# Performance work log

Measured on AMD Instinct MI355X. Metric: run time of the kernel, lower is better.

The kernel has to match this reference:

```python
import jax, jax.numpy as jnp
import numpy as np

B, N, M = 64, 1025, 1024          # N = M + 1 (node 0 is the zero-padding node)
TREE_FEAT = 96
QVEC = 95                          # sum(range(10)) + 10*5
IN_CH = TREE_FEAT + 32             # tree features + q_conv output
EPS = 1e-5


def _tree_conv(x, idx, W, b):
    # x: (B, C, N); idx: (B, 3M) child-triple indices into node axis
    g = jnp.take_along_axis(x, idx[:, None, :], axis=2)        # (B, C, 3M)
    Bn, C, L = g.shape
    g = g.reshape(Bn, C, L // 3, 3)                            # (B, C, M, 3)
    out = jnp.einsum('bcmk,ock->bom', g, W) + b[None, :, None] # Conv1d k=3 s=3
    zero = jnp.zeros((Bn, W.shape[0], 1), out.dtype)           # re-prepend zero node
    return jnp.concatenate([zero, out], axis=2)                # (B, O, M+1)


def _tree_norm(x):
    # TreeLayerNorm: per-sample mean/std over (channels, nodes); torch.std is unbiased
    mean = jnp.mean(x, axis=(1, 2), keepdims=True)
    std = jnp.std(x, axis=(1, 2), keepdims=True, ddof=1)
    return (x - mean) / (std + EPS)


def setup_inputs() -> dict:
    key = jax.random.key(0)
    ks = jax.random.split(key, 17)
    p = lambda k, s: jax.random.normal(k, s, dtype=jnp.float32) * 0.05
    return {
        'q_vecs': jax.random.normal(ks[0], (B, QVEC), dtype=jnp.float32),
        'trees': jax.random.normal(ks[1], (B, N, TREE_FEAT), dtype=jnp.float32),
        'idxes': jax.random.randint(ks[2], (B, 3 * M), 0, N),
        # q_conv: Linear(95,64) -> Linear(64,128) -> Linear(128,64) -> Linear(64,32)
        'Wq1': p(ks[3], (QVEC, 64)),  'bq1': jnp.zeros((64,), jnp.float32),
        'Wq2': p(ks[4], (64, 128)),   'bq2': jnp.zeros((128,), jnp.float32),
        'Wq3': p(ks[5], (128, 64)),   'bq3': jnp.zeros((64,), jnp.float32),
        'Wq4': p(ks[6], (64, 32)),    'bq4': jnp.zeros((32,), jnp.float32),
        # tree_conv kernels: (out, in, 3)
        'Wc1': p(ks[7], (512, IN_CH, 3)), 'bc1': jnp.zeros((512,), jnp.float32),
        'Wc2': p(ks[8], (256, 512, 3)),   'bc2': jnp.zeros((256,), jnp.float32),
        'Wc3': p(ks[9], (128, 256, 3)),   'bc3': jnp.zeros((128,), jnp.float32),
    }


def reference(q_vecs, trees, idxes,
              Wq1, bq1, Wq2, bq2, Wq3, bq3, Wq4, bq4,
              Wc1, bc1, Wc2, bc2, Wc3, bc3):
    # q_conv: 4 stacked linears (no nonlinearity between them in the source)
    q = q_vecs @ Wq1 + bq1
    q = q @ Wq2 + bq2
    q = q @ Wq3 + bq3
    q = q @ Wq4 + bq4                                    # (B, 32)

    Bn, Nn = trees.shape[:2]
    q_rep = jnp.broadcast_to(q[:, None, :], (Bn, Nn, q.shape[-1]))
    aug = jnp.concatenate([trees, q_rep], axis=2)        # (B, N, IN_CH)
    x = jnp.transpose(aug, (0, 2, 1))                    # (B, IN_CH, N)

    x = _tree_conv(x, idxes, Wc1, bc1)
    x = jax.nn.leaky_relu(_tree_norm(x), negative_slope=0.01)
    x = _tree_conv(x, idxes, Wc2, bc2)
    x = jax.nn.leaky_relu(_tree_norm(x), negative_slope=0.01)
    x = _tree_conv(x, idxes, Wc3, bc3)
    x = _tree_norm(x)
    return jnp.max(x, axis=2)                            # DynamicPooling -> (B, 128)
```

## Files before the change

kernel.cpp:

```cpp
#include <hip/hip_runtime.h>
#include <hip/hip_bf16.h>

typedef __attribute__((ext_vector_type(8))) short short8;
typedef __attribute__((ext_vector_type(4))) float f32x4;

#define EPSV 1e-5f

__device__ __forceinline__ float bf2f(ushort u){
  union { uint i; float f; } x; x.i = ((uint)u) << 16; return x.f;
}
__device__ __forceinline__ ushort f2bf(float f){
  union { float f; uint i; } x; x.f = f;
  uint r = (x.i + 0x7FFFu + ((x.i >> 16) & 1u)) >> 16;
  return (ushort)r;
}

__global__ void init_kernel(ushort* x1, float* stats, int* maxbuf){
  int i = blockIdx.x * 256 + threadIdx.x;
  if (i < 384)  stats[i] = 0.f;
  if (i < 8192) maxbuf[i] = 0;
  if (i < 32768){ int b = i >> 9, c = i & 511; x1[(size_t)b*1025*512 + c] = 0; }
}

__global__ void zero2_kernel(ushort* x2){
  int i = blockIdx.x * 256 + threadIdx.x;
  int b = i >> 8, c = i & 255;
  x2[(size_t)b*1025*256 + c] = 0;
}

__global__ void qconv_kernel(const float* __restrict__ qv,
    const float* __restrict__ W1, const float* __restrict__ b1,
    const float* __restrict__ W2, const float* __restrict__ b2,
    const float* __restrict__ W3, const float* __restrict__ b3,
    const float* __restrict__ W4, const float* __restrict__ b4,
    float* __restrict__ qout){
  __shared__ float v0[96], h1[64], h2[128], h3[64];
  int b = blockIdx.x, t = threadIdx.x;
  if (t < 95) v0[t] = qv[b*95 + t];
  __syncthreads();
  if (t < 64){ float s = b1[t]; for (int i=0;i<95;i++)  s += v0[i]*W1[i*64 + t];  h1[t]=s; }
  __syncthreads();
  if (t < 128){ float s = b2[t]; for (int i=0;i<64;i++)  s += h1[i]*W2[i*128 + t]; h2[t]=s; }
  __syncthreads();
  if (t < 64){ float s = b3[t]; for (int i=0;i<128;i++) s += h2[i]*W3[i*64 + t];  h3[t]=s; }
  __syncthreads();
  if (t < 32){ float s = b4[t]; for (int i=0;i<64;i++)  s += h3[i]*W4[i*32 + t];  qout[b*32 + t]=s; }
}

__global__ void aug_kernel(const float* __restrict__ trees, const float* __restrict__ q,
                           ushort* __restrict__ aug){
  int n = blockIdx.x;
  int b = blockIdx.y;
  int c = threadIdx.x;
  float v = (c < 96) ? trees[((size_t)b*1025 + n)*96 + c] : q[b*32 + (c - 96)];
  aug[(((size_t)b*1025 + n) << 7) + c] = f2bf(v);
}

__global__ void prepw_kernel(const float* __restrict__ wc, ushort* __restrict__ wt,
                             int O, int C){
  int i = blockIdx.x * 256 + threadIdx.x;
  int total = O * 3 * C;
  if (i >= total) return;
  int o  = i / (3*C);
  int K  = i - o*3*C;
  int kp = K / C;
  int c  = K - kp*C;
  wt[i] = f2bf(wc[(o*C + c)*3 + kp]);
}

template<int CIN, int GY, int TM, bool DO_MAX>
__global__ __launch_bounds__(256) void conv_kernel(
    const ushort* __restrict__ xin, const ushort* __restrict__ wt,
    const float* __restrict__ bias, const int* __restrict__ idxes,
    ushort* __restrict__ xout, float* __restrict__ stats, int* __restrict__ maxbuf){
  constexpr int K3    = 3 * CIN;
  constexpr int NT    = K3 / 32;
  constexpr int LOG2  = (CIN == 128) ? 7 : (CIN == 256) ? 8 : 9;
  constexpr int MT    = 1024 / TM;
  constexpr int MF    = TM / 32;
  constexpr int COUT  = GY * 128;
  constexpr int NWG   = MT * GY * 64;

  const int bid  = blockIdx.x;
  const int wu   = (bid & 7) * (NWG >> 3) + (bid >> 3);
  const int m0   = (wu % MT) * TM;
  const int rest = wu / MT;
  const int o0   = (rest % GY) * 128;
  const int b    = rest / GY;

  const int t = threadIdx.x;
  const int lane = t & 63, wid = t >> 6;
  const int WM = (wid & 1) * (TM/2), WO = (wid >> 1) * 64;
  const int fr = lane & 15, fg = lane >> 4;
  const int fc = (fg ^ ((fr >> 1) & 3)) * 8;

  __shared__ __align__(16) ushort As[2][TM][32];
  __shared__ __align__(16) ushort Bs[2][128][32];
  __shared__ int idx_s[3*TM];

  for (int i = t; i < 3*TM; i += 256) idx_s[i] = idxes[b*3072 + m0*3 + i];
  __syncthreads();

  const int rB = t >> 1, h = t & 1, sxB = (rB >> 1) & 3;
  const int pB0 = ((2*h)     ^ sxB) * 8;
  const int pB1 = ((2*h + 1) ^ sxB) * 8;
  const ushort* wrow = wt + (size_t)(o0 + rB) * K3 + h*16;

  const int rA  = (TM == 128) ? (t >> 1) : (t >> 2);
  const int qA  = (TM == 128) ? 0 : (t & 3);
  const int sxA = (rA >> 1) & 3;
  const int pA0 = (TM == 128) ? (((2*h) ^ sxA) * 8) : (((qA) ^ sxA) * 8);
  const int pA1 = ((2*h + 1) ^ sxA) * 8;
  const int aoff = (TM == 128) ? h*16 : qA*8;
  const int n0 = idx_s[rA*3 + 0], n1 = idx_s[rA*3 + 1], n2 = idx_s[rA*3 + 2];
  const ushort* xb  = xin + (size_t)b * 1025 * CIN;
  const ushort* pA0g = xb + (size_t)n0 * CIN + aoff;
  const ushort* pA1g = xb + (size_t)n1 * CIN + aoff;
  const ushort* pA2g = xb + (size_t)n2 * CIN + aoff;

  uint4 a00, a01, a10, a11, b00, b01, b10, b11;

  auto GLOAD0 = [&](int ch){
    const int k0 = ch * 32;
    const int kp = k0 >> LOG2;
    const int c0 = k0 - (kp << LOG2);
    const ushort* sa = ((kp == 0) ? pA0g : (kp == 1) ? pA1g : pA2g) + c0;
    a00 = *reinterpret_cast<const uint4*>(sa);
    if constexpr (TM == 128) a01 = *reinterpret_cast<const uint4*>(sa + 8);
    const ushort* sb = wrow + k0;
    b00 = *reinterpret_cast<const uint4*>(sb);
    b01 = *reinterpret_cast<const uint4*>(sb + 8);
  };
  auto GLOAD1 = [&](int ch){
    const int k0 = ch * 32;
    const int kp = k0 >> LOG2;
    const int c0 = k0 - (kp << LOG2);
    const ushort* sa = ((kp == 0) ? pA0g : (kp == 1) ? pA1g : pA2g) + c0;
    a10 = *reinterpret_cast<const uint4*>(sa);
    if constexpr (TM == 128) a11 = *reinterpret_cast<const uint4*>(sa + 8);
    const ushort* sb = wrow + k0;
    b10 = *reinterpret_cast<const uint4*>(sb);
    b11 = *reinterpret_cast<const uint4*>(sb + 8);
  };
  auto DSW0 = [&](int bf){
    *reinterpret_cast<uint4*>(&As[bf][rA][pA0]) = a00;
    if constexpr (TM == 128) *reinterpret_cast<uint4*>(&As[bf][rA][pA1]) = a01;
    *reinterpret_cast<uint4*>(&Bs[bf][rB][pB0]) = b00;
    *reinterpret_cast<uint4*>(&Bs[bf][rB][pB1]) = b01;
  };
  auto DSW1 = [&](int bf){
    *reinterpret_cast<uint4*>(&As[bf][rA][pA0]) = a10;
    if constexpr (TM == 128) *reinterpret_cast<uint4*>(&As[bf][rA][pA1]) = a11;
    *reinterpret_cast<uint4*>(&Bs[bf][rB][pB0]) = b10;
    *reinterpret_cast<uint4*>(&Bs[bf][rB][pB1]) = b11;
  };

  f32x4 acc[MF][4] = {};
  auto COMPUTE = [&](int cur){
    short8 af[MF], bf4[4];
    #pragma unroll
    for (int i = 0; i < MF; ++i)
      af[i] = *reinterpret_cast<const short8*>(&As[cur][WM + i*16 + fr][fc]);
    #pragma unroll
    for (int i = 0; i < 4; ++i)
      bf4[i] = *reinterpret_cast<const short8*>(&Bs[cur][WO + i*16 + fr][fc]);
    __builtin_amdgcn_s_setprio(1);
    #pragma unroll
    for (int mf = 0; mf < MF; ++mf)
      #pragma unroll
      for (int nf = 0; nf < 4; ++nf)
        acc[mf][nf] = __builtin_amdgcn_mfma_f32_16x16x32_bf16(af[mf], bf4[nf], acc[mf][nf], 0, 0, 0);
    __builtin_amdgcn_s_setprio(0);
  };

  GLOAD0(0);
  DSW0(0);
  GLOAD1(1);
  __syncthreads();

  for (int ch = 0; ch < NT; ch += 2){
    if (ch + 2 < NT) GLOAD0(ch + 2);
    COMPUTE(0);
    DSW1(1);
    __syncthreads();
    if (ch + 3 < NT) GLOAD1(ch + 3);
    COMPUTE(1);
    if (ch + 2 < NT){
      DSW0(0);
      __syncthreads();
    }
  }

  float bsv[4];
  #pragma unroll
  for (int nf = 0; nf < 4; ++nf) bsv[nf] = bias[o0 + WO + nf*16 + fr];
  float lsum = 0.f, lsq = 0.f;
  float cmax[4] = { -1e30f, -1e30f, -1e30f, -1e30f };
  #pragma unroll
  for (int mf = 0; mf < MF; ++mf)
    #pragma unroll
    for (int nf = 0; nf < 4; ++nf)
      #pragma unroll
      for (int i = 0; i < 4; ++i){
        float v = acc[mf][nf][i] + bsv[nf];
        lsum += v; lsq += v*v;
        if (DO_MAX) cmax[nf] = fmaxf(cmax[nf], v);
        else acc[mf][nf][i] = v;
      }
  #pragma unroll
  for (int off = 1; off < 64; off <<= 1){
    lsum += __shfl_xor(lsum, off);
    lsq  += __shfl_xor(lsq,  off);
  }
  if (lane == 0){
    atomicAdd(&stats[b],      lsum);
    atomicAdd(&stats[64 + b], lsq);
  }
  if (DO_MAX){
    #pragma unroll
    for (int nf = 0; nf < 4; ++nf){
      float v = cmax[nf];
      v = fmaxf(v, __shfl_xor(v, 16));
      v = fmaxf(v, __shfl_xor(v, 32));
      if (lane < 16)
        atomicMax(&maxbuf[b*COUT + o0 + WO + nf*16 + fr], __float_as_int(v));
    }
  } else {
    ushort* orow = xout + ((size_t)(b*1025 + 1 + m0 + WM + fg*4))*COUT + o0 + WO + fr;
    #pragma unroll
    for (int mf = 0; mf < MF; ++mf)
      #pragma unroll
      for (int i = 0; i < 4; ++i){
        ushort* pr = orow + (size_t)(mf*16 + i)*COUT;
        #pragma unroll
        for (int nf = 0; nf < 4; ++nf)
          pr[nf*16] = f2bf(acc[mf][nf][i]);
      }
  }
}

__global__ void norm_kernel(ushort* __restrict__ x, const float* __restrict__ st,
                            float cnt, int nvec_per_b){
  int b = blockIdx.y;
  int j = blockIdx.x * 256 + threadIdx.x;
  if (j >= nvec_per_b) return;
  float sum = st[b], sq = st[64 + b];
  float mean = sum / cnt;
  float var  = fmaxf((sq - sum*sum/cnt) / (cnt - 1.f), 0.f);
  float rs   = 1.f / (sqrtf(var) + EPSV);
  ushort* p = x + ((size_t)b * nvec_per_b + j) * 8;
  union { uint4 v; ushort u[8]; } d;
  d.v = *reinterpret_cast<const uint4*>(p);
  #pragma unroll
  for (int k = 0; k < 8; ++k){
    float f = bf2f(d.u[k]);
    f = (f - mean) * rs;
    f = (f >= 0.f) ? f : 0.01f * f;
    d.u[k] = f2bf(f);
  }
  *reinterpret_cast<uint4*>(p) = d.v;
}

__global__ void final_kernel(const int* __restrict__ maxbuf, const float* __restrict__ st,
                             float* __restrict__ out){
  int i = blockIdx.x * 256 + threadIdx.x;
  int b = i >> 7;
  const float cnt = 131200.f;
  float sum = st[b], sq = st[64 + b];
  float mean = sum / cnt;
  float var  = fmaxf((sq - sum*sum/cnt) / (cnt - 1.f), 0.f);
  float rs   = 1.f / (sqrtf(var) + EPSV);
  out[i] = (__int_as_float(maxbuf[i]) - mean) * rs;
}

static constexpr size_t SZ_X1  = (size_t)64*1025*512*2;
static constexpr size_t SZ_X2  = (size_t)64*1025*256*2;
static constexpr size_t OFF_X1 = 0;
static constexpr size_t OFF_X2 = OFF_X1 + SZ_X1;
static constexpr size_t OFF_AUG = OFF_X2;
static constexpr size_t OFF_WT1 = OFF_X2 + SZ_X2;
static constexpr size_t OFF_WT2 = OFF_WT1 + (size_t)512*384*2;
static constexpr size_t OFF_WT3 = OFF_WT2 + (size_t)256*1536*2;
static constexpr size_t OFF_Q   = OFF_WT3 + (size_t)128*768*2;
static constexpr size_t OFF_ST  = OFF_Q + (size_t)64*32*4;
static constexpr size_t OFF_MAX = OFF_ST + (size_t)384*4;

extern "C" void kernel_launch(void* const* d_in, const int* in_sizes, int n_in,
                              void* d_out, int out_size, void* d_ws, size_t ws_size,
                              hipStream_t stream){
  const float* q_vecs = (const float*)d_in[0];
  const float* trees  = (const float*)d_in[1];
  const int*   idxes  = (const int*)  d_in[2];
  const float* Wq1 = (const float*)d_in[3];  const float* bq1 = (const float*)d_in[4];
  const float* Wq2 = (const float*)d_in[5];  const float* bq2 = (const float*)d_in[6];
  const float* Wq3 = (const float*)d_in[7];  const float* bq3 = (const float*)d_in[8];
  const float* Wq4 = (const float*)d_in[9];  const float* bq4 = (const float*)d_in[10];
  const float* Wc1 = (const float*)d_in[11]; const float* bc1 = (const float*)d_in[12];
  const float* Wc2 = (const float*)d_in[13]; const float* bc2 = (const float*)d_in[14];
  const float* Wc3 = (const float*)d_in[15]; const float* bc3 = (const float*)d_in[16];
  float* out = (float*)d_out;
  char* ws = (char*)d_ws;

  ushort* x1    = (ushort*)(ws + OFF_X1);
  ushort* x2    = (ushort*)(ws + OFF_X2);
  ushort* aug   = (ushort*)(ws + OFF_AUG);
  ushort* wt1   = (ushort*)(ws + OFF_WT1);
  ushort* wt2   = (ushort*)(ws + OFF_WT2);
  ushort* wt3   = (ushort*)(ws + OFF_WT3);
  float*  qbuf  = (float*) (ws + OFF_Q);
  float*  stats = (float*) (ws + OFF_ST);
  int*    maxb  = (int*)   (ws + OFF_MAX);

  init_kernel<<<128, 256, 0, stream>>>(x1, stats, maxb);
  qconv_kernel<<<64, 128, 0, stream>>>(q_vecs, Wq1,bq1, Wq2,bq2, Wq3,bq3, Wq4,bq4, qbuf);
  aug_kernel<<<dim3(1025, 64), 128, 0, stream>>>(trees, qbuf, aug);
  prepw_kernel<<<(512*384 + 255)/256, 256, 0, stream>>>(Wc1, wt1, 512, 128);
  prepw_kernel<<<(256*1536 + 255)/256, 256, 0, stream>>>(Wc2, wt2, 256, 512);
  prepw_kernel<<<(128*768 + 255)/256, 256, 0, stream>>>(Wc3, wt3, 128, 256);

  conv_kernel<128, 4, 128, false><<<2048, 256, 0, stream>>>(aug, wt1, bc1, idxes, x1, stats +   0, nullptr);
  zero2_kernel<<<64, 256, 0, stream>>>(x2);
  norm_kernel<<<dim3((65600 + 255)/256, 64), 256, 0, stream>>>(x1, stats +   0, 524800.f, 65600);
  conv_kernel<512, 2, 128, false><<<1024, 256, 0, stream>>>(x1,  wt2, bc2, idxes, x2, stats + 128, nullptr);
  norm_kernel<<<dim3((32800 + 255)/256, 64), 256, 0, stream>>>(x2, stats + 128, 262400.f, 32800);
  conv_kernel<256, 1, 64, true ><<<1024, 256, 0, stream>>>(x2,  wt3, bc3, idxes, nullptr, stats + 256, maxb);
  final_kernel<<<32, 256, 0, stream>>>(maxb, stats + 256, out);
}
```

Baseline: 271.8 us.

## Fuse tree-norm and leaky-ReLU into next conv's gather; stage output stores via LDS

The standalone norm kernels are removed. Each following conv now computes mean and rstd from the previous layer's stats and applies normalize plus leaky-ReLU to the gathered bf16 A tile before writing it to shared memory. This avoids a full read-modify-write pass over the x1 and x2 activations. The cost is redundant normalization ALU work, since each node is gathered several times and by every output-channel group. The epilogue also stages bf16 outputs through a shared-memory buffer, unioned with the A/B tiles, so global stores are written as coalesced row chunks instead of scattered 2-byte writes.

```diff
diff --git a/kernel.cpp b/kernel.cpp
--- a/kernel.cpp
+++ b/kernel.cpp
@@ -13,6 +13,17 @@
   union { float f; uint i; } x; x.f = f;
   uint r = (x.i + 0x7FFFu + ((x.i >> 16) & 1u)) >> 16;
   return (ushort)r;
+}
+__device__ __forceinline__ uint4 nrm8(uint4 v, float nmr, float rs){
+  union { uint4 u; ushort s[8]; } x; x.u = v;
+  #pragma unroll
+  for (int k = 0; k < 8; ++k){
+    float f = bf2f(x.s[k]);
+    f = f * rs + nmr;
+    f = fmaxf(f, 0.01f * f);
+    x.s[k] = f2bf(f);
+  }
+  return x.u;
 }
 
 __global__ void init_kernel(ushort* x1, float* stats, int* maxbuf){
@@ -68,11 +79,12 @@
   wt[i] = f2bf(wc[(o*C + c)*3 + kp]);
 }
 
-template<int CIN, int GY, int TM, bool DO_MAX>
+template<int CIN, int GY, int TM, bool DO_MAX, bool NORM>
 __global__ __launch_bounds__(256) void conv_kernel(
     const ushort* __restrict__ xin, const ushort* __restrict__ wt,
     const float* __restrict__ bias, const int* __restrict__ idxes,
-    ushort* __restrict__ xout, float* __restrict__ stats, int* __restrict__ maxbuf){
+    ushort* __restrict__ xout, float* __restrict__ stats, int* __restrict__ maxbuf,
+    const float* __restrict__ stats_prev, float cnt){
   constexpr int K3    = 3 * CIN;
   constexpr int NT    = K3 / 32;
   constexpr int LOG2  = (CIN == 128) ? 7 : (CIN == 256) ? 8 : 9;
@@ -88,14 +100,25 @@
   const int o0   = (rest % GY) * 128;
   const int b    = rest / GY;
 
+  float nmr = 0.f, rsc = 0.f;
+  if (NORM){
+    float sum = stats_prev[b], sq = stats_prev[64 + b];
+    float mean = sum / cnt;
+    float var  = fmaxf((sq - sum*sum/cnt) / (cnt - 1.f), 0.f);
+    rsc = 1.f / (sqrtf(var) + EPSV);
+    nmr = -mean * rsc;
+  }
+
   const int t = threadIdx.x;
   const int lane = t & 63, wid = t >> 6;
   const int WM = (wid & 1) * (TM/2), WO = (wid >> 1) * 64;
   const int fr = lane & 15, fg = lane >> 4;
   const int fc = (fg ^ ((fr >> 1) & 3)) * 8;
 
-  __shared__ __align__(16) ushort As[2][TM][32];
-  __shared__ __align__(16) ushort Bs[2][128][32];
+  __shared__ __align__(16) union {
+    struct { ushort A[2][TM][32]; ushort B[2][128][32]; } s;
+    ushort stage[TM][132];
+  } sh;
   __shared__ int idx_s[3*TM];
 
   for (int i = t; i < 3*TM; i += 256) idx_s[i] = idxes[b*3072 + m0*3 + i];
@@ -113,7 +136,7 @@
   const int pA1 = ((2*h + 1) ^ sxA) * 8;
   const int aoff = (TM == 128) ? h*16 : qA*8;
   const int n0 = idx_s[rA*3 + 0], n1 = idx_s[rA*3 + 1], n2 = idx_s[rA*3 + 2];
-  const ushort* xb  = xin + (size_t)b * 1025 * CIN;
+  const ushort* xb   = xin + (size_t)b * 1025 * CIN;
   const ushort* pA0g = xb + (size_t)n0 * CIN + aoff;
   const ushort* pA1g = xb + (size_t)n1 * CIN + aoff;
   const ushort* pA2g = xb + (size_t)n2 * CIN + aoff;
@@ -143,16 +166,24 @@
     b11 = *reinterpret_cast<const uint4*>(sb + 8);
   };
   auto DSW0 = [&](int bf){
-    *reinterpret_cast<uint4*>(&As[bf][rA][pA0]) = a00;
-    if constexpr (TM == 128) *reinterpret_cast<uint4*>(&As[bf][rA][pA1]) = a01;
-    *reinterpret_cast<uint4*>(&Bs[bf][rB][pB0]) = b00;
-    *reinterpret_cast<uint4*>(&Bs[bf][rB][pB1]) = b01;
+    uint4 w0 = NORM ? nrm8(a00, nmr, rsc) : a00;
+    *reinterpret_cast<uint4*>(&sh.s.A[bf][rA][pA0]) = w0;
+    if constexpr (TM == 128){
+      uint4 w1 = NORM ? nrm8(a01, nmr, rsc) : a01;
+      *reinterpret_cast<uint4*>(&sh.s.A[bf][rA][pA1]) = w1;
+    }
+    *reinterpret_cast<uint4*>(&sh.s.B[bf][rB][pB0]) = b00;
+    *reinterpret_cast<uint4*>(&sh.s.B[bf][rB][pB1]) = b01;
   };
   auto DSW1 = [&](int bf){
-    *reinterpret_cast<uint4*>(&As[bf][rA][pA0]) = a10;
-    if constexpr (TM == 128) *reinterpret_cast<uint4*>(&As[bf][rA][pA1]) = a11;
-    *reinterpret_cast<uint4*>(&Bs[bf][rB][pB0]) = b10;
-    *reinterpret_cast<uint4*>(&Bs[bf][rB][pB1]) = b11;
+    uint4 w0 = NORM ? nrm8(a10, nmr, rsc) : a10;
+    *reinterpret_cast<uint4*>(&sh.s.A[bf][rA][pA0]) = w0;
+    if constexpr (TM == 128){
+      uint4 w1 = NORM ? nrm8(a11, nmr, rsc) : a11;
+      *reinterpret_cast<uint4*>(&sh.s.A[bf][rA][pA1]) = w1;
+    }
+    *reinterpret_cast<uint4*>(&sh.s.B[bf][rB][pB0]) = b10;
+    *reinterpret_cast<uint4*>(&sh.s.B[bf][rB][pB1]) = b11;
   };
 
   f32x4 acc[MF][4] = {};
@@ -160,10 +191,10 @@
     short8 af[MF], bf4[4];
     #pragma unroll
     for (int i = 0; i < MF; ++i)
-      af[i] = *reinterpret_cast<const short8*>(&As[cur][WM + i*16 + fr][fc]);
+      af[i] = *reinterpret_cast<const short8*>(&sh.s.A[cur][WM + i*16 + fr][fc]);
     #pragma unroll
     for (int i = 0; i < 4; ++i)
-      bf4[i] = *reinterpret_cast<const short8*>(&Bs[cur][WO + i*16 + fr][fc]);
+      bf4[i] = *reinterpret_cast<const short8*>(&sh.s.B[cur][WO + i*16 + fr][fc]);
     __builtin_amdgcn_s_setprio(1);
     #pragma unroll
     for (int mf = 0; mf < MF; ++mf)
@@ -226,39 +257,23 @@
         atomicMax(&maxbuf[b*COUT + o0 + WO + nf*16 + fr], __float_as_int(v));
     }
   } else {
-    ushort* orow = xout + ((size_t)(b*1025 + 1 + m0 + WM + fg*4))*COUT + o0 + WO + fr;
+    __syncthreads();
     #pragma unroll
     for (int mf = 0; mf < MF; ++mf)
       #pragma unroll
-      for (int i = 0; i < 4; ++i){
-        ushort* pr = orow + (size_t)(mf*16 + i)*COUT;
+      for (int nf = 0; nf < 4; ++nf)
         #pragma unroll
-        for (int nf = 0; nf < 4; ++nf)
-          pr[nf*16] = f2bf(acc[mf][nf][i]);
-      }
-  }
-}
-
-__global__ void norm_kernel(ushort* __restrict__ x, const float* __restrict__ st,
-                            float cnt, int nvec_per_b){
-  int b = blockIdx.y;
-  int j = blockIdx.x * 256 + threadIdx.x;
-  if (j >= nvec_per_b) return;
-  float sum = st[b], sq = st[64 + b];
-  float mean = sum / cnt;
-  float var  = fmaxf((sq - sum*sum/cnt) / (cnt - 1.f), 0.f);
-  float rs   = 1.f / (sqrtf(var) + EPSV);
-  ushort* p = x + ((size_t)b * nvec_per_b + j) * 8;
-  union { uint4 v; ushort u[8]; } d;
-  d.v = *reinterpret_cast<const uint4*>(p);
-  #pragma unroll
-  for (int k = 0; k < 8; ++k){
-    float f = bf2f(d.u[k]);
-    f = (f - mean) * rs;
-    f = (f >= 0.f) ? f : 0.01f * f;
-    d.u[k] = f2bf(f);
-  }
-  *reinterpret_cast<uint4*>(p) = d.v;
+        for (int i = 0; i < 4; ++i)
+          sh.stage[WM + mf*16 + fg*4 + i][WO + nf*16 + fr] = f2bf(acc[mf][nf][i]);
+    __syncthreads();
+    #pragma unroll
+    for (int it = 0; it < TM/8; ++it){
+      int row = it*8 + (t >> 5);
+      int col = (t & 31) * 4;
+      uint2 v = *reinterpret_cast<const uint2*>(&sh.stage[row][col]);
+      *reinterpret_cast<uint2*>(xout + ((size_t)(b*1025 + 1 + m0 + row))*COUT + o0 + col) = v;
+    }
+  }
 }
 
 __global__ void final_kernel(const int* __restrict__ maxbuf, const float* __restrict__ st,
@@ -318,11 +333,12 @@
   prepw_kernel<<<(256*1536 + 255)/256, 256, 0, stream>>>(Wc2, wt2, 256, 512);
   prepw_kernel<<<(128*768 + 255)/256, 256, 0, stream>>>(Wc3, wt3, 128, 256);
 
-  conv_kernel<128, 4, 128, false><<<2048, 256, 0, stream>>>(aug, wt1, bc1, idxes, x1, stats +   0, nullptr);
+  conv_kernel<128, 4, 128, false, false><<<2048, 256, 0, stream>>>(
+      aug, wt1, bc1, idxes, x1, stats + 0, nullptr, nullptr, 1.f);
   zero2_kernel<<<64, 256, 0, stream>>>(x2);
-  norm_kernel<<<dim3((65600 + 255)/256, 64), 256, 0, stream>>>(x1, stats +   0, 524800.f, 65600);
-  conv_kernel<512, 2, 128, false><<<1024, 256, 0, stream>>>(x1,  wt2, bc2, idxes, x2, stats + 128, nullptr);
-  norm_kernel<<<dim3((32800 + 255)/256, 64), 256, 0, stream>>>(x2, stats + 128, 262400.f, 32800);
-  conv_kernel<256, 1, 64, true ><<<1024, 256, 0, stream>>>(x2,  wt3, bc3, idxes, nullptr, stats + 256, maxb);
+  conv_kernel<512, 2, 128, false, true><<<1024, 256, 0, stream>>>(
+      x1, wt2, bc2, idxes, x2, stats + 128, nullptr, stats + 0, 524800.f);
+  conv_kernel<256, 1, 64, true, true><<<1024, 256, 0, stream>>>(
+      x2, wt3, bc3, idxes, nullptr, stats + 256, maxb, stats + 128, 262400.f);
   final_kernel<<<32, 256, 0, stream>>>(maxb, stats + 256, out);
 }
```

New measurement: 266.8 us. Within noise of the previous version (-1.8%).
